# Kernel tuning notes

Measured on AMD Instinct MI355X. Metric: run time of the kernel, lower is better.

## Reference

```python
import jax, jax.numpy as jnp
import numpy as np

N = 50000   # total nodes in batch
E = 640000  # directed edges
G = 64      # graphs in batch
D_IN = 128
D_H = 128
D_OUT = 10


def _glorot(key, shape):
    fan_in = shape[0]
    return jax.random.normal(key, shape, dtype=jnp.float32) / np.sqrt(fan_in)


def setup_inputs() -> dict:
    key = jax.random.key(0)
    ks = jax.random.split(key, 10)
    x = jax.random.normal(ks[0], (N, D_IN), dtype=jnp.float32)
    src = jax.random.randint(ks[1], (E,), 0, N, dtype=jnp.int32)
    dst = jax.random.randint(ks[2], (E,), 0, N, dtype=jnp.int32)
    batch = jnp.sort(jax.random.randint(ks[3], (N,), 0, G, dtype=jnp.int32))
    return {
        "x": x, "src": src, "dst": dst, "batch": batch,
        "W1": _glorot(ks[4], (D_IN, D_H)), "b1": jnp.zeros((D_H,), jnp.float32),
        "W2": _glorot(ks[5], (D_H, D_H)), "b2": jnp.zeros((D_H,), jnp.float32),
        "W3": _glorot(ks[6], (D_H, D_H)), "b3": jnp.zeros((D_H,), jnp.float32),
        "Wl": _glorot(ks[7], (D_H, D_OUT)), "bl": jnp.zeros((D_OUT,), jnp.float32),
    }


def gcn_conv(x, W, b, src, dst):
    """PyG GCNConv: add self-loops, symmetric deg^-1/2 normalization,
    linear transform, scatter-sum aggregation at dst, plus bias."""
    n = x.shape[0]
    loops = jnp.arange(n, dtype=src.dtype)
    s = jnp.concatenate([src, loops])  # [E+N]
    d = jnp.concatenate([dst, loops])
    deg = jax.ops.segment_sum(jnp.ones_like(d, dtype=x.dtype), d, num_segments=n)
    dinv = jnp.where(deg > 0, jax.lax.rsqrt(deg), 0.0)
    norm = dinv[s] * dinv[d]                        # [E+N]
    h = x @ W                                       # [N, D]
    out = jax.ops.segment_sum(h[s] * norm[:, None], d, num_segments=n)
    return out + b


def reference(x, src, dst, batch, W1, b1, W2, b2, W3, b3, Wl, bl):
    n = x.shape[0]
    h = jax.nn.relu(gcn_conv(x, W1, b1, src, dst))
    # dropout is a no-op in eval mode
    h = jax.nn.relu(gcn_conv(h, W2, b2, src, dst))
    h = gcn_conv(h, W3, b3, src, dst)
    # global_mean_pool over graph ids
    sums = jax.ops.segment_sum(h, batch, num_segments=G)            # [G, D]
    counts = jax.ops.segment_sum(jnp.ones((n,), h.dtype), batch, num_segments=G)
    pooled = sums / jnp.maximum(counts, 1.0)[:, None]
    logits = pooled @ Wl + bl                                       # [G, D_OUT]
    return jax.nn.log_softmax(logits, axis=1)
```

## Files before the change

kernel.cpp:

```cpp
#include <hip/hip_runtime.h>


constexpr int D = 128;
constexpr int DOUT = 10;
constexpr int PSPLIT = 8;
constexpr int BSH = 3;
constexpr int BCAP = 192;
constexpr int CPAD = 16;

using short8  = __attribute__((ext_vector_type(8))) short;
using float4v = __attribute__((ext_vector_type(4))) float;
using f32x2   = __attribute__((ext_vector_type(2))) float;

__device__ __forceinline__ ushort f2bf(float f) {
  uint u = __float_as_uint(f);
  return (ushort)((u + 0x7fffu + ((u >> 16) & 1u)) >> 16);
}
__device__ __forceinline__ float bf2f(ushort s) {
  return __uint_as_float(((uint)s) << 16);
}
__device__ __forceinline__ float bfhi(uint u) { return __uint_as_float(u & 0xffff0000u); }


__global__ void init_kernel(int* __restrict__ bcnt, int total) {
  int i = blockIdx.x * blockDim.x + threadIdx.x;
  if (i < total) bcnt[i] = 0;
}

__global__ void binfill_kernel(const int* __restrict__ src, const int* __restrict__ dst,
    int* __restrict__ bcnt, uint* __restrict__ buck, int e) {
  int i = blockIdx.x * blockDim.x + threadIdx.x;
  if (i >= e) return;
  int d = dst[i], s = src[i];
  int b = d >> BSH;
  int pos = atomicAdd(&bcnt[b * CPAD], 1);
  if (pos < BCAP)
    buck[(size_t)b * BCAP + pos] = (uint)s | ((uint)(d & ((1 << BSH) - 1)) << 16);
}

__global__ __launch_bounds__(256) void countb_kernel(const uint* __restrict__ buck,
    const int* __restrict__ bcnt, int* __restrict__ cnt, float* __restrict__ dinv,
    int* __restrict__ bsum, int n) {
  __shared__ int lc[256];
  const int base = blockIdx.x * 256;
  const int m = min(256, n - base);
  lc[threadIdx.x] = 0;
  __syncthreads();
  const int b0 = base >> BSH;
  #pragma unroll
  for (int bb = 0; bb < (256 >> BSH); ++bb) {
    int b = b0 + bb;
    if ((b << BSH) >= n) break;
    int c = min(bcnt[b * CPAD], BCAP);
    for (int i = threadIdx.x; i < c; i += 256)
      atomicAdd(&lc[(bb << BSH) + (int)(buck[(size_t)b * BCAP + i] >> 16)], 1);
  }
  __syncthreads();
  int v = lc[threadIdx.x];
  if ((int)threadIdx.x < m) {
    cnt[base + threadIdx.x] = v;
    dinv[base + threadIdx.x] = rsqrtf((float)(v + 1));
  }
  __shared__ int sd[256];
  sd[threadIdx.x] = ((int)threadIdx.x < m) ? v : 0;
  __syncthreads();
  for (int off = 128; off > 0; off >>= 1) {
    if (threadIdx.x < (unsigned)off) sd[threadIdx.x] += sd[threadIdx.x + off];
    __syncthreads();
  }
  if (threadIdx.x == 0) bsum[blockIdx.x] = sd[0];
}

__global__ __launch_bounds__(1024) void scan2_kernel(const int* __restrict__ bsum,
    int* __restrict__ boff, int nb, int* __restrict__ rowptr, int n) {
  __shared__ int sd[1024];
  int v = ((int)threadIdx.x < nb) ? bsum[threadIdx.x] : 0;
  sd[threadIdx.x] = v;
  __syncthreads();
  for (int off = 1; off < 1024; off <<= 1) {
    int t = (threadIdx.x >= (unsigned)off) ? sd[threadIdx.x - off] : 0;
    __syncthreads();
    sd[threadIdx.x] += t;
    __syncthreads();
  }
  if ((int)threadIdx.x < nb) boff[threadIdx.x] = sd[threadIdx.x] - v;
  if ((int)threadIdx.x == nb - 1) rowptr[n] = sd[threadIdx.x];
}

__global__ __launch_bounds__(256) void scatter_kernel(const uint* __restrict__ buck,
    const int* __restrict__ bcnt, const int* __restrict__ cnt,
    const int* __restrict__ boff, int* __restrict__ rowptr,
    const float* __restrict__ dinv, uint* __restrict__ epk, int n) {
  __shared__ int sd[256];
  __shared__ int lcur[256];
  const int base = blockIdx.x * 256;
  const int m = min(256, n - base);
  const int i = base + (int)threadIdx.x;
  int v = (i < n) ? cnt[i] : 0;
  sd[threadIdx.x] = v;
  __syncthreads();
  for (int off = 1; off < 256; off <<= 1) {
    int t = (threadIdx.x >= (unsigned)off) ? sd[threadIdx.x - off] : 0;
    __syncthreads();
    sd[threadIdx.x] += t;
    __syncthreads();
  }
  int rp = boff[blockIdx.x] + sd[threadIdx.x] - v;
  if (i < n) {
    rowptr[i] = rp;
    lcur[threadIdx.x] = rp;
  }
  __syncthreads();
  const int b0 = base >> BSH;
  #pragma unroll
  for (int bb = 0; bb < (256 >> BSH); ++bb) {
    int b = b0 + bb;
    if ((b << BSH) >= n) break;
    int c = min(bcnt[b * CPAD], BCAP);
    for (int j = threadIdx.x; j < c; j += 256) {
      uint rec = buck[(size_t)b * BCAP + j];
      int dl = (int)(rec >> 16);
      int s = (int)(rec & 0xffffu);
      int d = (b << BSH) + dl;
      int slot = atomicAdd(&lcur[(bb << BSH) + dl], 1);
      epk[slot] = (uint)s | ((uint)f2bf(dinv[s] * dinv[d]) << 16);
    }
  }
}

__global__ __launch_bounds__(256) void prepw_kernel(const float* __restrict__ W1,
    const float* __restrict__ W2, const float* __restrict__ W3, ushort* __restrict__ Wp) {
  const float* W = (blockIdx.y == 0) ? W1 : (blockIdx.y == 1) ? W2 : W3;
  ushort* Wpo = Wp + (size_t)blockIdx.y * 2048 * 8;
  int idx = blockIdx.x * 256 + threadIdx.x;
  int cf = idx >> 8, kk = (idx >> 6) & 3, lane = idx & 63;
  int k0 = kk * 32 + (lane >> 4) * 8;
  int c = cf * 16 + (lane & 15);
  uint p[4];
  #pragma unroll
  for (int h = 0; h < 4; ++h) {
    ushort lo = f2bf(W[(k0 + 2 * h) * D + c]);
    ushort hi = f2bf(W[(k0 + 2 * h + 1) * D + c]);
    p[h] = (uint)lo | ((uint)hi << 16);
  }
  uint4 w = make_uint4(p[0], p[1], p[2], p[3]);
  *(uint4*)(Wpo + idx * 8) = w;
}

template<bool F32>
__global__ __launch_bounds__(256) void gemm_mfma(const void* __restrict__ Ain,
    const ushort* __restrict__ Wp, uchar* __restrict__ out, int n) {
  __shared__ ushort wl[2048 * 8];
  const int tid = threadIdx.x;
  #pragma unroll
  for (int i = 0; i < 8; ++i) {
    int idx = tid + i * 256;
    *(uint4*)(&wl[idx * 8]) = *(const uint4*)(Wp + idx * 8);
  }
  __syncthreads();
  const int w = tid >> 6, lane = tid & 63;
  const int row0 = blockIdx.x * 64 + w * 16;
  int arow = row0 + (lane & 15);
  if (arow >= n) arow = n - 1;

  short8 a[4];
  if constexpr (F32) {
    const float* abase = (const float*)Ain + (size_t)arow * D + ((lane >> 4) * 8);
    #pragma unroll
    for (int kk = 0; kk < 4; ++kk) {
      float4 f0 = *(const float4*)(abase + kk * 32);
      float4 f1 = *(const float4*)(abase + kk * 32 + 4);
      short8 v;
      v[0] = (short)f2bf(f0.x); v[1] = (short)f2bf(f0.y);
      v[2] = (short)f2bf(f0.z); v[3] = (short)f2bf(f0.w);
      v[4] = (short)f2bf(f1.x); v[5] = (short)f2bf(f1.y);
      v[6] = (short)f2bf(f1.z); v[7] = (short)f2bf(f1.w);
      a[kk] = v;
    }
  } else {
    const ushort* abase = (const ushort*)Ain + (size_t)arow * D + ((lane >> 4) * 8);
    #pragma unroll
    for (int kk = 0; kk < 4; ++kk) a[kk] = *(const short8*)(abase + kk * 32);
  }

  float4v acc[8] = {};
  #pragma unroll
  for (int kk = 0; kk < 4; ++kk) {
    #pragma unroll
    for (int cf = 0; cf < 8; ++cf) {
      short8 b = *(const short8*)(&wl[((cf * 4 + kk) * 64 + lane) * 8]);
      acc[cf] = __builtin_amdgcn_mfma_f32_16x16x32_bf16(a[kk], b, acc[cf], 0, 0, 0);
    }
  }
  const int crow = row0 + (lane >> 4) * 4;
  const int ccol = lane & 15;
  #pragma unroll
  for (int cf = 0; cf < 8; ++cf) {
    #pragma unroll
    for (int r = 0; r < 4; ++r) {
      if (crow + r < n) {
        int enc = __builtin_amdgcn_cvt_pk_fp8_f32(acc[cf][r], acc[cf][r], 0, false);
        out[(size_t)(crow + r) * D + cf * 16 + ccol] = (uchar)(enc & 0xff);
      }
    }
  }
}

__global__ __launch_bounds__(256) void agg_kernel(const uchar* __restrict__ h8,
    const int* __restrict__ rowptr, const uint* __restrict__ epk,
    const float* __restrict__ dinv, const float* __restrict__ bias,
    ushort* __restrict__ out, int n, int relu) {
  int node = (int)((blockIdx.x * blockDim.x + threadIdx.x) >> 6);
  if (node >= n) return;
  const int lane = threadIdx.x & 63;
  const int sub = lane >> 5;
  const int li = lane & 31;
  const int beg = rowptr[node], end = rowptr[node + 1];
  float a0 = 0.f, a1 = 0.f, a2 = 0.f, a3 = 0.f;
  for (int e = beg; e < end; e += 16) {
    uint mm[8], rr[8];
    #pragma unroll
    for (int k = 0; k < 8; ++k)
      mm[k] = epk[min(e + 2 * k + sub, end - 1)];
    #pragma unroll
    for (int k = 0; k < 8; ++k)
      rr[k] = *(const uint*)(h8 + (size_t)(mm[k] & 0xffffu) * D + li * 4);
    #pragma unroll
    for (int k = 0; k < 8; ++k) {
      float wk = (e + 2 * k + sub < end) ? bfhi(mm[k]) : 0.f;
      f32x2 pa = __builtin_amdgcn_cvt_pk_f32_fp8(rr[k], false);
      f32x2 pb = __builtin_amdgcn_cvt_pk_f32_fp8(rr[k], true);
      a0 += pa[0] * wk;
      a1 += pa[1] * wk;
      a2 += pb[0] * wk;
      a3 += pb[1] * wk;
    }
  }
  a0 += __shfl_xor(a0, 32);
  a1 += __shfl_xor(a1, 32);
  a2 += __shfl_xor(a2, 32);
  a3 += __shfl_xor(a3, 32);
  const float di = dinv[node];
  const float dsq = di * di;
  uint sv = *(const uint*)(h8 + (size_t)node * D + li * 4);
  f32x2 sa = __builtin_amdgcn_cvt_pk_f32_fp8(sv, false);
  f32x2 sb = __builtin_amdgcn_cvt_pk_f32_fp8(sv, true);
  a0 += sa[0] * dsq;
  a1 += sa[1] * dsq;
  a2 += sb[0] * dsq;
  a3 += sb[1] * dsq;
  float4 bv = *(const float4*)(bias + li * 4);
  a0 += bv.x; a1 += bv.y; a2 += bv.z; a3 += bv.w;
  if (relu) {
    a0 = fmaxf(a0, 0.f); a1 = fmaxf(a1, 0.f);
    a2 = fmaxf(a2, 0.f); a3 = fmaxf(a3, 0.f);
  }
  if (sub == 0) {
    uint2 pk;
    pk.x = (uint)f2bf(a0) | ((uint)f2bf(a1) << 16);
    pk.y = (uint)f2bf(a2) | ((uint)f2bf(a3) << 16);
    *(uint2*)(out + (size_t)node * D + li * 4) = pk;
  }
}

__global__ __launch_bounds__(256) void pool1_kernel(const ushort* __restrict__ act,
    const int* __restrict__ batch, float* __restrict__ pp, int n) {
  const int g = blockIdx.x;
  const int sp = blockIdx.y;
  int lo = 0, hi = n;
  while (lo < hi) { int mid = (lo + hi) >> 1; if (batch[mid] < g) lo = mid + 1; else hi = mid; }
  const int start = lo;
  hi = n;
  while (lo < hi) { int mid = (lo + hi) >> 1; if (batch[mid] <= g) lo = mid + 1; else hi = mid; }
  const int end = lo;
  const int len = end - start;
  const int per = (len + PSPLIT - 1) / PSPLIT;
  const int i0 = start + sp * per;
  const int i1 = min(i0 + per, end);

  const int rt = threadIdx.x >> 4;
  const int ds = threadIdx.x & 15;
  float acc[8] = {};
  for (int i = i0 + rt; i < i1; i += 16) {
    short8 v = *(const short8*)(act + (size_t)i * D + ds * 8);
    #pragma unroll
    for (int e2 = 0; e2 < 8; ++e2) acc[e2] += bf2f((ushort)v[e2]);
  }
  __shared__ float sd[256][8];
  #pragma unroll
  for (int e2 = 0; e2 < 8; ++e2) sd[threadIdx.x][e2] = acc[e2];
  __syncthreads();
  if (threadIdx.x < 128) {
    int d = threadIdx.x;
    int slice = d >> 3, e2 = d & 7;
    float s = 0.f;
    #pragma unroll
    for (int k = 0; k < 16; ++k) s += sd[k * 16 + slice][e2];
    pp[((size_t)g * PSPLIT + sp) * D + d] = s;
  }
}

__global__ __launch_bounds__(640) void head_kernel(const float* __restrict__ pp,
    const int* __restrict__ batch, const float* __restrict__ Wl,
    const float* __restrict__ bl, float* __restrict__ out, int n, int g) {
  __shared__ float pooled[64 * D];
  __shared__ float cnts[64];
  __shared__ float lg[64][DOUT];
  const int tid = threadIdx.x;
  if (tid < g) {
    int gg = tid;
    int lo = 0, hi = n;
    while (lo < hi) { int mid = (lo + hi) >> 1; if (batch[mid] < gg) lo = mid + 1; else hi = mid; }
    int start = lo;
    hi = n;
    while (lo < hi) { int mid = (lo + hi) >> 1; if (batch[mid] <= gg) lo = mid + 1; else hi = mid; }
    cnts[gg] = fmaxf((float)(lo - start), 1.f);
  }
  __syncthreads();
  for (int idx = tid; idx < g * D; idx += 640) {
    int gg = idx >> 7, d = idx & 127;
    float s = 0.f;
    #pragma unroll
    for (int sp = 0; sp < PSPLIT; ++sp) s += pp[((size_t)gg * PSPLIT + sp) * D + d];
    pooled[idx] = s / cnts[gg];
  }
  __syncthreads();
  int gi = tid / DOUT, o = tid % DOUT;
  if (gi < g) {
    float acc = bl[o];
    for (int d = 0; d < D; ++d) acc += pooled[gi * D + d] * Wl[d * DOUT + o];
    lg[gi][o] = acc;
  }
  __syncthreads();
  if (gi < g) {
    float m = -1e30f;
    for (int j = 0; j < DOUT; ++j) m = fmaxf(m, lg[gi][j]);
    float s = 0.f;
    for (int j = 0; j < DOUT; ++j) s += expf(lg[gi][j] - m);
    out[gi * DOUT + o] = lg[gi][o] - m - logf(s);
  }
}


extern "C" void kernel_launch(void* const* d_in, const int* in_sizes, int n_in,
                              void* d_out, int out_size, void* d_ws, size_t ws_size,
                              hipStream_t stream) {
  const float* x   = (const float*)d_in[0];
  const int* src   = (const int*)d_in[1];
  const int* dst   = (const int*)d_in[2];
  const int* batch = (const int*)d_in[3];
  const float* W1  = (const float*)d_in[4];
  const float* b1  = (const float*)d_in[5];
  const float* W2  = (const float*)d_in[6];
  const float* b2  = (const float*)d_in[7];
  const float* W3  = (const float*)d_in[8];
  const float* b3  = (const float*)d_in[9];
  const float* Wl  = (const float*)d_in[10];
  const float* bl  = (const float*)d_in[11];
  float* out = (float*)d_out;

  const int n = in_sizes[0] / D;
  const int e = in_sizes[1];
  const int g = out_size / DOUT;

  char* p = (char*)d_ws;
  auto alloc = [&](size_t bytes) {
    char* r = p;
    p += (bytes + 255) & ~(size_t)255;
    return r;
  };
  const int nb = (n + 255) / 256;
  const int NB = (n + (1 << BSH) - 1) >> BSH;
  int* cnt      = (int*)alloc((size_t)n * 4);
  int* rowptr   = (int*)alloc((size_t)(n + 1) * 4);
  float* dinv   = (float*)alloc((size_t)n * 4);
  int* bsum     = (int*)alloc((size_t)nb * 4);
  int* boff     = (int*)alloc((size_t)nb * 4);
  int* bcnt     = (int*)alloc((size_t)NB * CPAD * 4);
  uint* buck    = (uint*)alloc((size_t)NB * BCAP * 4);
  uint* epk     = (uint*)alloc((size_t)e * 4);
  ushort* Wp    = (ushort*)alloc(3 * 2048 * 16);
  ushort* bfA   = (ushort*)alloc((size_t)n * D * 2);
  ushort* bfB   = (ushort*)alloc((size_t)n * D * 2);
  uchar* tmp8   = (uchar*)alloc((size_t)n * D);
  float* pp     = (float*)alloc((size_t)g * PSPLIT * D * 4);
  (void)ws_size;

  const int B = 256;
  const int gridE = (e + B - 1) / B;

  init_kernel<<<(NB * CPAD + B - 1) / B, B, 0, stream>>>(bcnt, NB * CPAD);
  binfill_kernel<<<gridE, B, 0, stream>>>(src, dst, bcnt, buck, e);
  countb_kernel<<<nb, B, 0, stream>>>(buck, bcnt, cnt, dinv, bsum, n);
  scan2_kernel<<<1, 1024, 0, stream>>>(bsum, boff, nb, rowptr, n);
  scatter_kernel<<<nb, B, 0, stream>>>(buck, bcnt, cnt, boff, rowptr, dinv, epk, n);
  prepw_kernel<<<dim3(8, 3), B, 0, stream>>>(W1, W2, W3, Wp);

  const int gemmGrid = (n + 63) / 64;
  const int aggGrid = (n * 64 + B - 1) / B;

  gemm_mfma<true><<<gemmGrid, B, 0, stream>>>(x, Wp, tmp8, n);
  agg_kernel<<<aggGrid, B, 0, stream>>>(tmp8, rowptr, epk, dinv, b1, bfB, n, 1);
  gemm_mfma<false><<<gemmGrid, B, 0, stream>>>(bfB, Wp + 2048 * 8, tmp8, n);
  agg_kernel<<<aggGrid, B, 0, stream>>>(tmp8, rowptr, epk, dinv, b2, bfA, n, 1);
  gemm_mfma<false><<<gemmGrid, B, 0, stream>>>(bfA, Wp + 2 * 2048 * 8, tmp8, n);
  agg_kernel<<<aggGrid, B, 0, stream>>>(tmp8, rowptr, epk, dinv, b3, bfB, n, 0);

  pool1_kernel<<<dim3(g, PSPLIT), B, 0, stream>>>(bfB, batch, pp, n);
  head_kernel<<<1, 640, 0, stream>>>(pp, batch, Wl, bl, out, n, g);
}
```

Before: 200.0 us.

## Fuse aggregation with following layer GEMM for layers one and two

Layers one and two now run a combined kernel: each 1024-thread block aggregates 16 nodes (one wave per node), stores the bf16 rows in shared memory, and then 8 waves run MFMA against the next layer's weights to write fp8 output directly. This drops two standalone GEMM launches and the bf16 intermediate write/read round trip. In exchange, half of each block's waves sit idle during the GEMM phase, the B operands are read from global memory instead of LDS, and the 1024-thread blocks may limit occupancy for the latency-bound gather.

```diff
diff --git a/kernel.cpp b/kernel.cpp
--- a/kernel.cpp
+++ b/kernel.cpp
@@ -94,7 +94,6 @@
   __shared__ int sd[256];
   __shared__ int lcur[256];
   const int base = blockIdx.x * 256;
-  const int m = min(256, n - base);
   const int i = base + (int)threadIdx.x;
   int v = (i < n) ? cnt[i] : 0;
   sd[threadIdx.x] = v;
@@ -147,8 +146,7 @@
   *(uint4*)(Wpo + idx * 8) = w;
 }
 
-template<bool F32>
-__global__ __launch_bounds__(256) void gemm_mfma(const void* __restrict__ Ain,
+__global__ __launch_bounds__(256) void gemm_mfma(const float* __restrict__ Ain,
     const ushort* __restrict__ Wp, uchar* __restrict__ out, int n) {
   __shared__ ushort wl[2048 * 8];
   const int tid = threadIdx.x;
@@ -164,23 +162,17 @@
   if (arow >= n) arow = n - 1;
 
   short8 a[4];
-  if constexpr (F32) {
-    const float* abase = (const float*)Ain + (size_t)arow * D + ((lane >> 4) * 8);
-    #pragma unroll
-    for (int kk = 0; kk < 4; ++kk) {
-      float4 f0 = *(const float4*)(abase + kk * 32);
-      float4 f1 = *(const float4*)(abase + kk * 32 + 4);
-      short8 v;
-      v[0] = (short)f2bf(f0.x); v[1] = (short)f2bf(f0.y);
-      v[2] = (short)f2bf(f0.z); v[3] = (short)f2bf(f0.w);
-      v[4] = (short)f2bf(f1.x); v[5] = (short)f2bf(f1.y);
-      v[6] = (short)f2bf(f1.z); v[7] = (short)f2bf(f1.w);
-      a[kk] = v;
-    }
-  } else {
-    const ushort* abase = (const ushort*)Ain + (size_t)arow * D + ((lane >> 4) * 8);
-    #pragma unroll
-    for (int kk = 0; kk < 4; ++kk) a[kk] = *(const short8*)(abase + kk * 32);
+  const float* abase = Ain + (size_t)arow * D + ((lane >> 4) * 8);
+  #pragma unroll
+  for (int kk = 0; kk < 4; ++kk) {
+    float4 f0 = *(const float4*)(abase + kk * 32);
+    float4 f1 = *(const float4*)(abase + kk * 32 + 4);
+    short8 v;
+    v[0] = (short)f2bf(f0.x); v[1] = (short)f2bf(f0.y);
+    v[2] = (short)f2bf(f0.z); v[3] = (short)f2bf(f0.w);
+    v[4] = (short)f2bf(f1.x); v[5] = (short)f2bf(f1.y);
+    v[6] = (short)f2bf(f1.z); v[7] = (short)f2bf(f1.w);
+    a[kk] = v;
   }
 
   float4v acc[8] = {};
@@ -206,17 +198,13 @@
   }
 }
 
-__global__ __launch_bounds__(256) void agg_kernel(const uchar* __restrict__ h8,
+__device__ __forceinline__ void agg_node(const uchar* __restrict__ h8,
     const int* __restrict__ rowptr, const uint* __restrict__ epk,
     const float* __restrict__ dinv, const float* __restrict__ bias,
-    ushort* __restrict__ out, int n, int relu) {
-  int node = (int)((blockIdx.x * blockDim.x + threadIdx.x) >> 6);
-  if (node >= n) return;
-  const int lane = threadIdx.x & 63;
-  const int sub = lane >> 5;
-  const int li = lane & 31;
+    int node, int sub, int li, int relu,
+    float& a0, float& a1, float& a2, float& a3) {
   const int beg = rowptr[node], end = rowptr[node + 1];
-  float a0 = 0.f, a1 = 0.f, a2 = 0.f, a3 = 0.f;
+  a0 = a1 = a2 = a3 = 0.f;
   for (int e = beg; e < end; e += 16) {
     uint mm[8], rr[8];
     #pragma unroll
@@ -255,6 +243,68 @@
     a0 = fmaxf(a0, 0.f); a1 = fmaxf(a1, 0.f);
     a2 = fmaxf(a2, 0.f); a3 = fmaxf(a3, 0.f);
   }
+}
+
+__global__ __launch_bounds__(1024) void aggemm_kernel(const uchar* __restrict__ h8,
+    const int* __restrict__ rowptr, const uint* __restrict__ epk,
+    const float* __restrict__ dinv, const float* __restrict__ bias,
+    const ushort* __restrict__ Wp, uchar* __restrict__ out8, int n) {
+  __shared__ ushort At[16][136];
+  const int wv = (int)(threadIdx.x >> 6);
+  const int lane = (int)(threadIdx.x & 63);
+  const int sub = lane >> 5;
+  const int li = lane & 31;
+  const int node = blockIdx.x * 16 + wv;
+  if (node < n) {
+    float a0, a1, a2, a3;
+    agg_node(h8, rowptr, epk, dinv, bias, node, sub, li, 1, a0, a1, a2, a3);
+    if (sub == 0) {
+      uint2 pk;
+      pk.x = (uint)f2bf(a0) | ((uint)f2bf(a1) << 16);
+      pk.y = (uint)f2bf(a2) | ((uint)f2bf(a3) << 16);
+      *(uint2*)(&At[wv][li * 4]) = pk;
+    }
+  } else if (sub == 0) {
+    *(uint2*)(&At[wv][li * 4]) = make_uint2(0, 0);
+  }
+  __syncthreads();
+  if (wv < 8) {
+    const int cf = wv;
+    const int r = lane & 15;
+    const int koff = (lane >> 4) * 8;
+    short8 a[4];
+    #pragma unroll
+    for (int kk = 0; kk < 4; ++kk)
+      a[kk] = *(const short8*)(&At[r][koff + kk * 32]);
+    float4v acc = {};
+    #pragma unroll
+    for (int kk = 0; kk < 4; ++kk) {
+      short8 b = *(const short8*)(Wp + (size_t)((cf * 4 + kk) * 64 + lane) * 8);
+      acc = __builtin_amdgcn_mfma_f32_16x16x32_bf16(a[kk], b, acc, 0, 0, 0);
+    }
+    const int crow = blockIdx.x * 16 + (lane >> 4) * 4;
+    const int ccol = lane & 15;
+    #pragma unroll
+    for (int r2 = 0; r2 < 4; ++r2) {
+      if (crow + r2 < n) {
+        int enc = __builtin_amdgcn_cvt_pk_fp8_f32(acc[r2], acc[r2], 0, false);
+        out8[(size_t)(crow + r2) * D + cf * 16 + ccol] = (uchar)(enc & 0xff);
+      }
+    }
+  }
+}
+
+__global__ __launch_bounds__(256) void agg_kernel(const uchar* __restrict__ h8,
+    const int* __restrict__ rowptr, const uint* __restrict__ epk,
+    const float* __restrict__ dinv, const float* __restrict__ bias,
+    ushort* __restrict__ out, int n, int relu) {
+  int node = (int)((blockIdx.x * blockDim.x + threadIdx.x) >> 6);
+  if (node >= n) return;
+  const int lane = threadIdx.x & 63;
+  const int sub = lane >> 5;
+  const int li = lane & 31;
+  float a0, a1, a2, a3;
+  agg_node(h8, rowptr, epk, dinv, bias, node, sub, li, relu, a0, a1, a2, a3);
   if (sub == 0) {
     uint2 pk;
     pk.x = (uint)f2bf(a0) | ((uint)f2bf(a1) << 16);
@@ -380,9 +430,9 @@
   uint* buck    = (uint*)alloc((size_t)NB * BCAP * 4);
   uint* epk     = (uint*)alloc((size_t)e * 4);
   ushort* Wp    = (ushort*)alloc(3 * 2048 * 16);
-  ushort* bfA   = (ushort*)alloc((size_t)n * D * 2);
   ushort* bfB   = (ushort*)alloc((size_t)n * D * 2);
-  uchar* tmp8   = (uchar*)alloc((size_t)n * D);
+  uchar* tmpA   = (uchar*)alloc((size_t)n * D);
+  uchar* tmpB   = (uchar*)alloc((size_t)n * D);
   float* pp     = (float*)alloc((size_t)g * PSPLIT * D * 4);
   (void)ws_size;
 
@@ -397,14 +447,15 @@
   prepw_kernel<<<dim3(8, 3), B, 0, stream>>>(W1, W2, W3, Wp);
 
   const int gemmGrid = (n + 63) / 64;
+  const int fuseGrid = (n + 15) / 16;
   const int aggGrid = (n * 64 + B - 1) / B;
 
-  gemm_mfma<true><<<gemmGrid, B, 0, stream>>>(x, Wp, tmp8, n);
-  agg_kernel<<<aggGrid, B, 0, stream>>>(tmp8, rowptr, epk, dinv, b1, bfB, n, 1);
-  gemm_mfma<false><<<gemmGrid, B, 0, stream>>>(bfB, Wp + 2048 * 8, tmp8, n);
-  agg_kernel<<<aggGrid, B, 0, stream>>>(tmp8, rowptr, epk, dinv, b2, bfA, n, 1);
-  gemm_mfma<false><<<gemmGrid, B, 0, stream>>>(bfA, Wp + 2 * 2048 * 8, tmp8, n);
-  agg_kernel<<<aggGrid, B, 0, stream>>>(tmp8, rowptr, epk, dinv, b3, bfB, n, 0);
+  gemm_mfma<<<gemmGrid, B, 0, stream>>>(x, Wp, tmpA, n);
+  aggemm_kernel<<<fuseGrid, 1024, 0, stream>>>(tmpA, rowptr, epk, dinv, b1,
+                                               Wp + 2048 * 8, tmpB, n);
+  aggemm_kernel<<<fuseGrid, 1024, 0, stream>>>(tmpB, rowptr, epk, dinv, b2,
+                                               Wp + 2 * 2048 * 8, tmpA, n);
+  agg_kernel<<<aggGrid, B, 0, stream>>>(tmpA, rowptr, epk, dinv, b3, bfB, n, 0);
 
   pool1_kernel<<<dim3(g, PSPLIT), B, 0, stream>>>(bfB, batch, pp, n);
   head_kernel<<<1, 640, 0, stream>>>(pp, batch, Wl, bl, out, n, g);
```

Result: faster. 194.1 us (-3.0%).
